# Kernel tuning notes

Hardware: AMD Instinct MI355X
Metric: run time of the kernel (lower is better)

## Reference

```python
import jax, jax.numpy as jnp
import numpy as np

N_NODES = 100000
N_EDGES = 640000
NIN = 128
NOUT = 128


def setup_inputs() -> dict:
    key = jax.random.key(0)
    ks = jax.random.split(key, 10)
    scale = 1.0 / np.sqrt(NIN)
    x = jax.random.normal(ks[0], (N_NODES, NIN), dtype=jnp.float32)
    edge_index = jax.random.randint(ks[1], (2, N_EDGES), 0, N_NODES, dtype=jnp.int64)
    edge_attr = jnp.zeros((N_EDGES, 1), dtype=jnp.float32)
    Wk = jax.random.uniform(ks[2], (NIN, NOUT), jnp.float32, -scale, scale)
    bk = jax.random.uniform(ks[3], (NOUT,), jnp.float32, -scale, scale)
    Wq = jax.random.uniform(ks[4], (NIN, NOUT), jnp.float32, -scale, scale)
    bq = jax.random.uniform(ks[5], (NOUT,), jnp.float32, -scale, scale)
    Wv = jax.random.uniform(ks[6], (NIN, NOUT), jnp.float32, -scale, scale)
    bv = jax.random.uniform(ks[7], (NOUT,), jnp.float32, -scale, scale)
    Wskip = jax.random.uniform(ks[8], (NIN, NOUT), jnp.float32, -scale, scale)
    bias = jax.random.uniform(ks[9], (NOUT,), jnp.float32, -scale, scale)
    return {
        "x": x, "edge_index": edge_index, "edge_attr": edge_attr,
        "Wk": Wk, "bk": bk, "Wq": Wq, "bq": bq,
        "Wv": Wv, "bv": bv, "Wskip": Wskip, "bias": bias,
    }


def reference(x, edge_index, edge_attr, Wk, bk, Wq, bq, Wv, bv, Wskip, bias):
    # PyG ResGatedGraphConv: out_i = W_skip x_i + b + sum_{j->i} sigmoid(k_i + q_j) * v_j
    # k = lin_key(x) (applied to dst), q = lin_query(x) (src), v = lin_value(x) (src)
    src, dst = edge_index[0], edge_index[1]
    k = x @ Wk + bk            # [N, NOUT]
    q = x @ Wq + bq            # [N, NOUT]
    v = x @ Wv + bv            # [N, NOUT]
    eta = jax.nn.sigmoid(k[dst] + q[src])   # [E, NOUT] per-edge gate
    msg = eta * v[src]                       # [E, NOUT]
    agg = jax.ops.segment_sum(msg, dst, num_segments=x.shape[0])  # [N, NOUT]
    return agg + x @ Wskip + bias
```

## Files before the change

### kernel.cpp

```cpp
#include <hip/hip_runtime.h>
#include <hip/hip_bf16.h>

typedef __bf16 v4bf __attribute__((ext_vector_type(4)));
typedef __bf16 v8bf __attribute__((ext_vector_type(8)));
typedef float  v16f __attribute__((ext_vector_type(16)));

#define LOG2E 1.44269504088896340736f

__device__ __forceinline__ unsigned short f2bf(float f) {
    union { float f; unsigned int u; } a; a.f = f;
    unsigned int r = a.u + 0x7FFFu + ((a.u >> 16) & 1u);
    return (unsigned short)(r >> 16);
}

__device__ __forceinline__ void unpack8(uint4 rawv, float* f) {
    unsigned int w[4] = { rawv.x, rawv.y, rawv.z, rawv.w };
    #pragma unroll
    for (int i = 0; i < 4; ++i) {
        f[2 * i]     = __uint_as_float(w[i] << 16);
        f[2 * i + 1] = __uint_as_float(w[i] & 0xFFFF0000u);
    }
}

__global__ __launch_bounds__(256) void prep_w_zero(
    const float* __restrict__ Wk, const float* __restrict__ Wq,
    const float* __restrict__ Wv, const float* __restrict__ Ws,
    unsigned short* __restrict__ Wt, int* __restrict__ deg, int N)
{
    int i = blockIdx.x * 256 + threadIdx.x;
    if (i < 65536) {
        int m = i >> 14;
        int r = i & 16383;
        int n = r >> 7, k = r & 127;
        const float* W = (m == 0) ? Wk : (m == 1) ? Wq : (m == 2) ? Wv : Ws;
        float scale = (m == 0) ? -LOG2E : (m == 1) ? LOG2E : 1.0f;
        Wt[i] = f2bf(W[k * 128 + n] * scale);
    }
    if (i < N) deg[i] = 0;
}

__global__ __launch_bounds__(1024, 4) void gemm_fused(
    const float* __restrict__ x, int N,
    const unsigned short* __restrict__ Wt,
    const float* __restrict__ bk, const float* __restrict__ bq,
    const float* __restrict__ bv, const float* __restrict__ bs,
    unsigned short* __restrict__ kws, unsigned short* __restrict__ qv,
    float* __restrict__ out)
{
    __shared__ __align__(16) unsigned short xs[32 * 132];
    const int t   = threadIdx.x;
    const int wid = t >> 6;
    const int m   = wid >> 2;
    const int ct  = wid & 3;
    const int l   = t & 63;
    const int col = ct * 32 + (l & 31);
    const int kb  = (l >> 5) * 8;

    v8bf b[8];
    {
        const unsigned short* wp = Wt + m * 16384 + col * 128 + kb;
        #pragma unroll
        for (int c = 0; c < 8; ++c) b[c] = *(const v8bf*)(wp + c * 16);
    }
    const float* bvec = (m == 0) ? bk : (m == 1) ? bq : (m == 2) ? bv : bs;
    const float bcol = bvec[col] * ((m == 0) ? -LOG2E : (m == 1) ? LOG2E : 1.0f);
    unsigned short* dst; int dstride;
    if (m == 0)      { dst = kws;      dstride = 128; }
    else if (m == 1) { dst = qv;       dstride = 256; }
    else             { dst = qv + 128; dstride = 256; }

    const int srow = t >> 5;
    const int sk4  = (t & 31) << 2;
    const int rowb = 4 * (l >> 5);

    const int ntiles = (N + 31) >> 5;
    int tile = blockIdx.x;
    if (tile >= ntiles) return;

    float4 stg = make_float4(0.f, 0.f, 0.f, 0.f);
    {
        int gr = tile * 32 + srow;
        if (gr < N) stg = *(const float4*)(x + (size_t)gr * 128 + sk4);
    }

    const unsigned short* ap = xs + (l & 31) * 132 + kb;

    while (true) {
        ushort4 pk;
        pk.x = f2bf(stg.x); pk.y = f2bf(stg.y);
        pk.z = f2bf(stg.z); pk.w = f2bf(stg.w);
        *(ushort4*)(xs + srow * 132 + sk4) = pk;
        __syncthreads();

        int next = tile + gridDim.x;
        if (next < ntiles) {
            int gr = next * 32 + srow;
            stg = (gr < N) ? *(const float4*)(x + (size_t)gr * 128 + sk4)
                           : make_float4(0.f, 0.f, 0.f, 0.f);
        }

        v16f acc = {};
        #pragma unroll
        for (int c = 0; c < 8; ++c) {
            v4bf a0 = *(const v4bf*)(ap + c * 16);
            v4bf a1 = *(const v4bf*)(ap + c * 16 + 4);
            v8bf a = __builtin_shufflevector(a0, a1, 0, 1, 2, 3, 4, 5, 6, 7);
            acc = __builtin_amdgcn_mfma_f32_32x32x16_bf16(a, b[c], acc, 0, 0, 0);
        }

        const int r0 = tile * 32 + rowb;
        if (m == 3) {
            #pragma unroll
            for (int reg = 0; reg < 16; ++reg) {
                int row = r0 + (reg & 3) + 8 * (reg >> 2);
                if (row < N) out[(size_t)row * 128 + col] = acc[reg] + bcol;
            }
        } else {
            #pragma unroll
            for (int reg = 0; reg < 16; ++reg) {
                int row = r0 + (reg & 3) + 8 * (reg >> 2);
                if (row < N) dst[(size_t)row * dstride + col] = f2bf(acc[reg] + bcol);
            }
        }

        tile = next;
        if (tile >= ntiles) break;
        __syncthreads();
    }
}


__global__ __launch_bounds__(256) void count_pos(
    const int* __restrict__ ei, int E, int* __restrict__ deg,
    int* __restrict__ pos)
{
    int e = blockIdx.x * 256 + threadIdx.x;
    if (e >= E) return;
    pos[e] = atomicAdd(&deg[ei[E + e]], 1);
}

__global__ __launch_bounds__(256) void scan_chunks(
    const int* __restrict__ deg, int N, int* __restrict__ rowStart,
    int* __restrict__ chunkTot)
{
    __shared__ int sums[256];
    const int t = threadIdx.x;
    const int base = blockIdx.x * 1024 + t * 4;
    int d0 = 0, d1 = 0, d2 = 0, d3 = 0;
    if (base + 3 < N) {
        int4 dd = *(const int4*)(deg + base);
        d0 = dd.x; d1 = dd.y; d2 = dd.z; d3 = dd.w;
    } else {
        if (base + 0 < N) d0 = deg[base + 0];
        if (base + 1 < N) d1 = deg[base + 1];
        if (base + 2 < N) d2 = deg[base + 2];
        if (base + 3 < N) d3 = deg[base + 3];
    }
    int tot = d0 + d1 + d2 + d3;
    sums[t] = tot;
    __syncthreads();
    #pragma unroll
    for (int off = 1; off < 256; off <<= 1) {
        int v = (t >= off) ? sums[t - off] : 0;
        __syncthreads();
        sums[t] += v;
        __syncthreads();
    }
    int excl = sums[t] - tot;
    if (base + 0 < N) rowStart[base + 0] = excl;
    if (base + 1 < N) rowStart[base + 1] = excl + d0;
    if (base + 2 < N) rowStart[base + 2] = excl + d0 + d1;
    if (base + 3 < N) rowStart[base + 3] = excl + d0 + d1 + d2;
    if (t == 255) chunkTot[blockIdx.x] = sums[255];
}

__global__ __launch_bounds__(256) void add_offsets(
    int* __restrict__ rowStart, const int* __restrict__ chunkTot,
    int N, int nChunks)
{
    __shared__ int s[128];
    const int t = threadIdx.x;
    if (t < 128) s[t] = (t < nChunks) ? chunkTot[t] : 0;
    __syncthreads();
    #pragma unroll
    for (int off = 1; off < 128; off <<= 1) {
        int u = 0;
        if (t < 128 && t >= off) u = s[t - off];
        __syncthreads();
        if (t < 128) s[t] += u;
        __syncthreads();
    }
    const int coff = (blockIdx.x == 0) ? 0 : s[blockIdx.x - 1];
    const int base = blockIdx.x * 1024 + t * 4;
    if (base + 3 < N) {
        int4 r = *(const int4*)(rowStart + base);
        r.x += coff; r.y += coff; r.z += coff; r.w += coff;
        *(int4*)(rowStart + base) = r;
    } else {
        #pragma unroll
        for (int j = 0; j < 4; ++j) {
            if (base + j < N) rowStart[base + j] += coff;
        }
    }
}

__global__ __launch_bounds__(256) void fill_csr(
    const int* __restrict__ ei, int E,
    const int* __restrict__ rowStart, const int* __restrict__ pos,
    int* __restrict__ elist)
{
    int e = blockIdx.x * 256 + threadIdx.x;
    if (e >= E) return;
    int s = ei[e];
    int d = ei[E + e];
    elist[rowStart[d] + pos[e]] = s;
}

__global__ __launch_bounds__(256, 4) void gather_agg(
    const int* __restrict__ rowStart, const int* __restrict__ deg,
    const int* __restrict__ elist,
    const unsigned short* __restrict__ kws,
    const unsigned short* __restrict__ qv,
    float* __restrict__ out, int N)
{
    int gid = blockIdx.x * 256 + threadIdx.x;
    int node = gid >> 4;
    if (node >= N) return;
    int fo = (gid & 15) << 3;

    float* orow = out + (size_t)node * 128 + fo;
    float4 o0 = *(const float4*)(orow);
    float4 o1 = *(const float4*)(orow + 4);
    uint4 kraw = *(const uint4*)(kws + (size_t)node * 128 + fo);
    const int p0 = rowStart[node];
    const int dg = deg[node];

    float nkf[8];
    unpack8(kraw, nkf);
    float acc[8] = {};

    const unsigned short* qvb = qv + fo;
    const int e = p0 + dg;

    for (int base = p0; base < e; base += 8) {
        int idx[8];
        #pragma unroll
        for (int s = 0; s < 8; ++s) {
            int pp = base + s;
            idx[s] = elist[pp < e ? pp : e - 1];
        }
        uint4 qr[8], vr[8];
        #pragma unroll
        for (int s = 0; s < 8; ++s) {
            const unsigned short* r = qvb + (idx[s] << 8);
            qr[s] = *(const uint4*)(r);
            vr[s] = *(const uint4*)(r + 128);
        }
        #pragma unroll
        for (int s = 0; s < 8; ++s) {
            if (base + s >= e) {
                vr[s].x = 0u; vr[s].y = 0u; vr[s].z = 0u; vr[s].w = 0u;
            }
            float qf[8], vf[8];
            unpack8(qr[s], qf);
            unpack8(vr[s], vf);
            #pragma unroll
            for (int j = 0; j < 8; ++j) {
                float ex = __builtin_amdgcn_exp2f(nkf[j] - qf[j]);
                acc[j] = fmaf(__builtin_amdgcn_rcpf(1.0f + ex), vf[j], acc[j]);
            }
        }
    }

    o0.x += acc[0]; o0.y += acc[1]; o0.z += acc[2]; o0.w += acc[3];
    o1.x += acc[4]; o1.y += acc[5]; o1.z += acc[6]; o1.w += acc[7];
    *(float4*)(orow)     = o0;
    *(float4*)(orow + 4) = o1;
}

extern "C" void kernel_launch(void* const* d_in, const int* in_sizes, int n_in,
                              void* d_out, int out_size, void* d_ws, size_t ws_size,
                              hipStream_t stream) {
    const float* x    = (const float*)d_in[0];
    const int*   ei   = (const int*)d_in[1];
    const float* Wk   = (const float*)d_in[3];
    const float* bk   = (const float*)d_in[4];
    const float* Wq   = (const float*)d_in[5];
    const float* bq   = (const float*)d_in[6];
    const float* Wv   = (const float*)d_in[7];
    const float* bv   = (const float*)d_in[8];
    const float* Ws   = (const float*)d_in[9];
    const float* bias = (const float*)d_in[10];

    const int N = in_sizes[0] / 128;
    const int E = in_sizes[1] / 2;
    float* out = (float*)d_out;

    unsigned short* kws = (unsigned short*)d_ws;
    unsigned short* qv  = kws + (size_t)N * 128;
    int* deg      = (int*)(qv + (size_t)N * 256);
    int* rowStart = deg + N;
    int* chunkTot = rowStart + N;
    int* pos      = chunkTot + 128;
    int* elist    = pos + E;
    unsigned short* Wt = (unsigned short*)(elist + E);

    const int nChunks = (N + 1023) / 1024;

    prep_w_zero<<<512, 256, 0, stream>>>(Wk, Wq, Wv, Ws, Wt, deg, N);
    gemm_fused<<<1024, 1024, 0, stream>>>(
        x, N, Wt, bk, bq, bv, bias, kws, qv, out);

    count_pos<<<(E + 255) / 256, 256, 0, stream>>>(ei, E, deg, pos);
    scan_chunks<<<nChunks, 256, 0, stream>>>(deg, N, rowStart, chunkTot);
    add_offsets<<<nChunks, 256, 0, stream>>>(rowStart, chunkTot, N, nChunks);
    fill_csr<<<(E + 255) / 256, 256, 0, stream>>>(ei, E, rowStart, pos, elist);

    gather_agg<<<((size_t)N * 16 + 255) / 256, 256, 0, stream>>>(
        rowStart, deg, elist, kws, qv, out, N);
}
```

Measured before the change: 268.9 us.

## Fuse degree counting into GEMM kernel and make gather kernel grid-stride

Moves the per-edge atomic degree count into the start of the fused GEMM kernel, which removes one kernel launch and lets the atomics overlap with the GEMM. The gather/aggregate kernel becomes a persistent grid-stride loop over nodes with a fixed 1024-block grid. Its per-iteration edge batch drops from 8 to 4, which lowers register pressure but leaves fewer loads in flight per thread. The GEMM blocks now do atomic work before they start tiling, which may delay the GEMM.

After: 260.4 us. 1.03x faster.

```diff
diff --git a/kernel.cpp b/kernel.cpp
--- a/kernel.cpp
+++ b/kernel.cpp
@@ -4,6 +4,8 @@
 typedef __bf16 v4bf __attribute__((ext_vector_type(4)));
 typedef __bf16 v8bf __attribute__((ext_vector_type(8)));
 typedef float  v16f __attribute__((ext_vector_type(16)));
+typedef float  f4v  __attribute__((ext_vector_type(4)));
+typedef unsigned int u4v __attribute__((ext_vector_type(4)));
 
 #define LOG2E 1.44269504088896340736f
 
@@ -13,8 +15,7 @@
     return (unsigned short)(r >> 16);
 }
 
-__device__ __forceinline__ void unpack8(uint4 rawv, float* f) {
-    unsigned int w[4] = { rawv.x, rawv.y, rawv.z, rawv.w };
+__device__ __forceinline__ void unpack8v(u4v w, float* f) {
     #pragma unroll
     for (int i = 0; i < 4; ++i) {
         f[2 * i]     = __uint_as_float(w[i] << 16);
@@ -45,8 +46,14 @@
     const float* __restrict__ bk, const float* __restrict__ bq,
     const float* __restrict__ bv, const float* __restrict__ bs,
     unsigned short* __restrict__ kws, unsigned short* __restrict__ qv,
-    float* __restrict__ out)
-{
+    float* __restrict__ out,
+    const int* __restrict__ ei, int E,
+    int* __restrict__ deg, int* __restrict__ pos)
+{
+    for (int e = blockIdx.x * 1024 + threadIdx.x; e < E; e += 1024 * 1024) {
+        pos[e] = atomicAdd(&deg[ei[E + e]], 1);
+    }
+
     __shared__ __align__(16) unsigned short xs[32 * 132];
     const int t   = threadIdx.x;
     const int wid = t >> 6;
@@ -129,15 +136,6 @@
     }
 }
 
-
-__global__ __launch_bounds__(256) void count_pos(
-    const int* __restrict__ ei, int E, int* __restrict__ deg,
-    int* __restrict__ pos)
-{
-    int e = blockIdx.x * 256 + threadIdx.x;
-    if (e >= E) return;
-    pos[e] = atomicAdd(&deg[ei[E + e]], 1);
-}
 
 __global__ __launch_bounds__(256) void scan_chunks(
     const int* __restrict__ deg, int N, int* __restrict__ rowStart,
@@ -211,9 +209,7 @@
 {
     int e = blockIdx.x * 256 + threadIdx.x;
     if (e >= E) return;
-    int s = ei[e];
-    int d = ei[E + e];
-    elist[rowStart[d] + pos[e]] = s;
+    elist[rowStart[ei[E + e]] + pos[e]] = ei[e];
 }
 
 __global__ __launch_bounds__(256, 4) void gather_agg(
@@ -223,59 +219,59 @@
     const unsigned short* __restrict__ qv,
     float* __restrict__ out, int N)
 {
-    int gid = blockIdx.x * 256 + threadIdx.x;
-    int node = gid >> 4;
-    if (node >= N) return;
-    int fo = (gid & 15) << 3;
-
-    float* orow = out + (size_t)node * 128 + fo;
-    float4 o0 = *(const float4*)(orow);
-    float4 o1 = *(const float4*)(orow + 4);
-    uint4 kraw = *(const uint4*)(kws + (size_t)node * 128 + fo);
-    const int p0 = rowStart[node];
-    const int dg = deg[node];
-
-    float nkf[8];
-    unpack8(kraw, nkf);
-    float acc[8] = {};
-
+    const int grp = threadIdx.x >> 4;
+    const int fo  = (threadIdx.x & 15) << 3;
+    const int gstride = gridDim.x * 16;
     const unsigned short* qvb = qv + fo;
-    const int e = p0 + dg;
-
-    for (int base = p0; base < e; base += 8) {
-        int idx[8];
-        #pragma unroll
-        for (int s = 0; s < 8; ++s) {
-            int pp = base + s;
-            idx[s] = elist[pp < e ? pp : e - 1];
-        }
-        uint4 qr[8], vr[8];
-        #pragma unroll
-        for (int s = 0; s < 8; ++s) {
-            const unsigned short* r = qvb + (idx[s] << 8);
-            qr[s] = *(const uint4*)(r);
-            vr[s] = *(const uint4*)(r + 128);
-        }
-        #pragma unroll
-        for (int s = 0; s < 8; ++s) {
-            if (base + s >= e) {
-                vr[s].x = 0u; vr[s].y = 0u; vr[s].z = 0u; vr[s].w = 0u;
-            }
-            float qf[8], vf[8];
-            unpack8(qr[s], qf);
-            unpack8(vr[s], vf);
-            #pragma unroll
-            for (int j = 0; j < 8; ++j) {
-                float ex = __builtin_amdgcn_exp2f(nkf[j] - qf[j]);
-                acc[j] = fmaf(__builtin_amdgcn_rcpf(1.0f + ex), vf[j], acc[j]);
-            }
-        }
-    }
-
-    o0.x += acc[0]; o0.y += acc[1]; o0.z += acc[2]; o0.w += acc[3];
-    o1.x += acc[4]; o1.y += acc[5]; o1.z += acc[6]; o1.w += acc[7];
-    *(float4*)(orow)     = o0;
-    *(float4*)(orow + 4) = o1;
+
+    for (int node = blockIdx.x * 16 + grp; node < N; node += gstride) {
+        float* orow = out + (size_t)node * 128 + fo;
+        f4v o0 = *(const f4v*)(orow);
+        f4v o1 = *(const f4v*)(orow + 4);
+        u4v kraw = *(const u4v*)(kws + (size_t)node * 128 + fo);
+        const int p0 = rowStart[node];
+        const int dg = deg[node];
+        const int e  = p0 + dg;
+        const int eL = e - 1;
+
+        float nkf[8];
+        unpack8v(kraw, nkf);
+        float acc[8] = {};
+
+        for (int base = p0; base < e; base += 4) {
+            int idx[4];
+            #pragma unroll
+            for (int s = 0; s < 4; ++s) {
+                int pp = base + s;
+                idx[s] = elist[pp < e ? pp : eL];
+            }
+            u4v qr[4], vr[4];
+            #pragma unroll
+            for (int s = 0; s < 4; ++s) {
+                const unsigned short* r = qvb + (idx[s] << 8);
+                qr[s] = *(const u4v*)(r);
+                vr[s] = *(const u4v*)(r + 128);
+            }
+            #pragma unroll
+            for (int s = 0; s < 4; ++s) {
+                u4v vv = vr[s];
+                if (base + s >= e) { vv[0] = 0u; vv[1] = 0u; vv[2] = 0u; vv[3] = 0u; }
+                float qf[8], vf[8];
+                unpack8v(qr[s], qf);
+                unpack8v(vv, vf);
+                #pragma unroll
+                for (int j = 0; j < 8; ++j) {
+                    float ex = __builtin_amdgcn_exp2f(nkf[j] - qf[j]);
+                    acc[j] = fmaf(__builtin_amdgcn_rcpf(1.0f + ex), vf[j], acc[j]);
+                }
+            }
+        }
+
+        o0[0] += acc[0]; o0[1] += acc[1]; o0[2] += acc[2]; o0[3] += acc[3];
+        o1[0] += acc[4]; o1[1] += acc[5]; o1[2] += acc[6]; o1[3] += acc[7];
+        *(f4v*)(orow)     = o0;
+        *(f4v*)(orow + 4) = o1;
+    }
 }
 
 extern "C" void kernel_launch(void* const* d_in, const int* in_sizes, int n_in,
@@ -309,13 +305,12 @@
 
     prep_w_zero<<<512, 256, 0, stream>>>(Wk, Wq, Wv, Ws, Wt, deg, N);
     gemm_fused<<<1024, 1024, 0, stream>>>(
-        x, N, Wt, bk, bq, bv, bias, kws, qv, out);
-
-    count_pos<<<(E + 255) / 256, 256, 0, stream>>>(ei, E, deg, pos);
+        x, N, Wt, bk, bq, bv, bias, kws, qv, out, ei, E, deg, pos);
+
     scan_chunks<<<nChunks, 256, 0, stream>>>(deg, N, rowStart, chunkTot);
     add_offsets<<<nChunks, 256, 0, stream>>>(rowStart, chunkTot, N, nChunks);
     fill_csr<<<(E + 255) / 256, 256, 0, stream>>>(ei, E, rowStart, pos, elist);
 
-    gather_agg<<<((size_t)N * 16 + 255) / 256, 256, 0, stream>>>(
+    gather_agg<<<1024, 256, 0, stream>>>(
         rowStart, deg, elist, kws, qv, out, N);
 }
```
